# Performance work log

Measured on AMD Instinct MI355X. Metric: run time of the kernel, lower is better.

Reference implementation:

```python
import jax, jax.numpy as jnp
import numpy as np

N_E = 1024
E_DIM = 64


def setup_inputs() -> dict:
    key = jax.random.key(0)
    k_z, k_emb = jax.random.split(key)
    z = jax.random.normal(k_z, (8, 16, 32, 32, E_DIM), dtype=jnp.float32)
    embeddings = jax.random.normal(k_emb, (N_E, E_DIM), dtype=jnp.float32) * 0.02
    return {"z": z, "embeddings": embeddings}


def reference(z, embeddings):
    # flatten all leading dims: [B*T*H*W, e_dim]
    zf = z.reshape(-1, z.shape[-1])
    # squared L2 distance: ||z||^2 + ||e||^2 - 2 z.e  -> [tokens, n_e]
    d = (jnp.sum(zf ** 2, axis=1, keepdims=True)
         + jnp.sum(embeddings ** 2, axis=1)[None, :]
         - 2.0 * jnp.einsum('bd,nd->bn', zf, embeddings))
    idx = jnp.argmin(d, axis=1)
    z_q = embeddings[idx].reshape(z.shape)
    idx = idx.reshape(z.shape[:-1])
    return z_q, idx
```

## Files before the change

kernel.cpp:

```cpp
#include <hip/hip_runtime.h>

typedef short short8 __attribute__((ext_vector_type(8)));
typedef float f32x4 __attribute__((ext_vector_type(4)));

#define NTOK (8 * 16 * 32 * 32)
#define NE 1024
#define ED 64
#define TPB 256
#define MBLK 128
#define NMF 2
#define WKEY (1 << 18)
#define SCALE (-131072.0f)

__device__ __forceinline__ unsigned short bf16_rtne(float f) {
    unsigned u = __float_as_uint(f);
    return (unsigned short)((u + 0x7FFFu + ((u >> 16) & 1u)) >> 16);
}
__device__ __forceinline__ float bf16_to_f32(unsigned short h) {
    return __uint_as_float(((unsigned)h) << 16);
}

__device__ float exact_dist(const float* __restrict__ z, const float* __restrict__ emb,
                            int t, int e) {
    const float* zt = z + (size_t)t * ED;
    const float* ep = emb + (size_t)e * ED;
    float r0 = 0.f, r1 = 0.f, r2 = 0.f, r3 = 0.f;
    float r4 = 0.f, r5 = 0.f, r6 = 0.f, r7 = 0.f;
    for (int d = 0; d < ED; d += 8) {
        r0 += zt[d + 0] * zt[d + 0];
        r1 += zt[d + 1] * zt[d + 1];
        r2 += zt[d + 2] * zt[d + 2];
        r3 += zt[d + 3] * zt[d + 3];
        r4 += zt[d + 4] * zt[d + 4];
        r5 += zt[d + 5] * zt[d + 5];
        r6 += zt[d + 6] * zt[d + 6];
        r7 += zt[d + 7] * zt[d + 7];
    }
    float s1 = ((r0 + r1) + (r2 + r3)) + ((r4 + r5) + (r6 + r7));
    float q0 = 0.f, q1 = 0.f, q2 = 0.f, q3 = 0.f;
    float q4 = 0.f, q5 = 0.f, q6 = 0.f, q7 = 0.f;
    for (int d = 0; d < ED; d += 8) {
        float v0 = ep[d + 0], v1 = ep[d + 1], v2 = ep[d + 2], v3 = ep[d + 3];
        float v4 = ep[d + 4], v5 = ep[d + 5], v6 = ep[d + 6], v7 = ep[d + 7];
        q0 += v0 * v0; q1 += v1 * v1; q2 += v2 * v2; q3 += v3 * v3;
        q4 += v4 * v4; q5 += v5 * v5; q6 += v6 * v6; q7 += v7 * v7;
    }
    float s2 = ((q0 + q1) + (q2 + q3)) + ((q4 + q5) + (q6 + q7));
    float a0 = 0.f, a1 = 0.f, a2 = 0.f, a3 = 0.f;
    for (int d = 0; d < ED; d += 4) {
        a0 = fmaf(zt[d + 0], ep[d + 0], a0);
        a1 = fmaf(zt[d + 1], ep[d + 1], a1);
        a2 = fmaf(zt[d + 2], ep[d + 2], a2);
        a3 = fmaf(zt[d + 3], ep[d + 3], a3);
    }
    float g = (a0 + a1) + (a2 + a3);
    return (s1 + s2) - 2.0f * g;
}

__global__ __launch_bounds__(128) void vq_prep(
    const float* __restrict__ emb,
    unsigned short* __restrict__ bfH,
    unsigned short* __restrict__ bfL,
    float* __restrict__ s2s)
{
    const int f = blockIdx.x * 128 + threadIdx.x;
    const int col = f & 15;
    const int quad = (f >> 4) & 3;
    const int kb = (f >> 6) & 1;
    const int nt = f >> 7;
    const int e = nt * 16 + col;
    const int k0 = kb * 32 + quad * 8;

    const float* p = emb + (size_t)e * ED + k0;
    float4 v0 = *(const float4*)p;
    float4 v1 = *(const float4*)(p + 4);
    float vs[8] = {v0.x, v0.y, v0.z, v0.w, v1.x, v1.y, v1.z, v1.w};
    short8 h, l;
#pragma unroll
    for (int j = 0; j < 8; ++j) {
        float x = vs[j] * SCALE;
        unsigned short hb = bf16_rtne(x);
        float hf = bf16_to_f32(hb);
        unsigned short lb = bf16_rtne(x - hf);
        h[j] = (short)hb;
        l[j] = (short)lb;
    }
    *(short8*)&bfH[(size_t)f * 8] = h;
    *(short8*)&bfL[(size_t)f * 8] = l;

    if (f < 4096) {
        const int row = f >> 2;
        const float4* rp = (const float4*)(emb + (size_t)row * ED + (f & 3) * 16);
        float4 a = rp[0], b = rp[1], c = rp[2], d = rp[3];
        float s = a.x * a.x + a.y * a.y + a.z * a.z + a.w * a.w
                + b.x * b.x + b.y * b.y + b.z * b.z + b.w * b.w
                + c.x * c.x + c.y * c.y + c.z * c.z + c.w * c.w
                + d.x * d.x + d.y * d.y + d.z * d.z + d.w * d.w;
        s += __shfl_xor(s, 1);
        s += __shfl_xor(s, 2);
        if ((f & 3) == 0) s2s[row] = s * 65536.0f;
    }
}

__global__ void __launch_bounds__(TPB)
__attribute__((amdgpu_waves_per_eu(4, 4))) vq_main(
    const float* __restrict__ z,
    const float* __restrict__ emb,
    const unsigned short* __restrict__ bfH,
    const unsigned short* __restrict__ bfL,
    const float* __restrict__ s2s_g,
    float* __restrict__ zq_out,
    float* __restrict__ idx_out)
{
    __shared__ float s2L[NE];
    __shared__ int idx_lds[MBLK];
    __shared__ uint4 Bbuf[2][256];

    const int tid = threadIdx.x;
    const int lane = tid & 63;
    const int wv = __builtin_amdgcn_readfirstlane(tid >> 6);
    const int col = lane & 15;
    const int quad = lane >> 4;
    const int blockTok = blockIdx.x * MBLK;

    for (int i = tid; i < NE; i += TPB) s2L[i] = s2s_g[i];

    const uint4* src = (const uint4*)(tid < 128 ? bfH : bfL);
    const int chunk = tid & 127;
    const int dstc = (tid >> 7) * 128 + chunk;

    short8 Ah[NMF][2], Al[NMF][2];
#pragma unroll
    for (int mf = 0; mf < NMF; ++mf) {
#pragma unroll
        for (int kf = 0; kf < 2; ++kf) {
            const float* zp = z + (size_t)(blockTok + wv * 32 + mf * 16 + col) * ED
                              + kf * 32 + quad * 8;
            float4 v0 = *(const float4*)zp;
            float4 v1 = *(const float4*)(zp + 4);
            float vs[8] = {v0.x, v0.y, v0.z, v0.w, v1.x, v1.y, v1.z, v1.w};
            short8 h, l;
#pragma unroll
            for (int j = 0; j < 8; ++j) {
                float x = vs[j];
                unsigned short hb = bf16_rtne(x);
                float hf = bf16_to_f32(hb);
                unsigned short lb = bf16_rtne(x - hf);
                h[j] = (short)hb;
                l[j] = (short)lb;
            }
            Ah[mf][kf] = h;
            Al[mf][kf] = l;
        }
    }

    int aK[NMF][4], bK[NMF][4];
#pragma unroll
    for (int mf = 0; mf < NMF; ++mf)
#pragma unroll
        for (int r = 0; r < 4; ++r) { aK[mf][r] = 0x7FFFFFFF; bK[mf][r] = 0x7FFFFFFF; }

    Bbuf[0][dstc] = src[chunk];
    __syncthreads();

    int p = 0;
    for (int nt = 0; nt < 64; ++nt) {
        uint4 nv;
        if (nt < 63) nv = src[(nt + 1) * 128 + chunk];

        const short8* bp = (const short8*)Bbuf[p];
        short8 Bh0 = bp[lane];
        short8 Bh1 = bp[64 + lane];
        short8 Bl0 = bp[128 + lane];
        short8 Bl1 = bp[192 + lane];

        const float s2v = s2L[nt * 16 + col];
        const int e = nt * 16 + col;
#pragma unroll
        for (int mf = 0; mf < NMF; ++mf) {
            f32x4 cc = {s2v, s2v, s2v, s2v};
            cc = __builtin_amdgcn_mfma_f32_16x16x32_bf16(Ah[mf][0], Bh0, cc, 0, 0, 0);
            cc = __builtin_amdgcn_mfma_f32_16x16x32_bf16(Ah[mf][1], Bh1, cc, 0, 0, 0);
            cc = __builtin_amdgcn_mfma_f32_16x16x32_bf16(Al[mf][0], Bh0, cc, 0, 0, 0);
            cc = __builtin_amdgcn_mfma_f32_16x16x32_bf16(Al[mf][1], Bh1, cc, 0, 0, 0);
            cc = __builtin_amdgcn_mfma_f32_16x16x32_bf16(Ah[mf][0], Bl0, cc, 0, 0, 0);
            cc = __builtin_amdgcn_mfma_f32_16x16x32_bf16(Ah[mf][1], Bl1, cc, 0, 0, 0);
#pragma unroll
            for (int r = 0; r < 4; ++r) {
                int key = ((int)cc[r]) * 1024 + e;
                int t1 = min(aK[mf][r], key);
                bK[mf][r] = min(bK[mf][r], max(aK[mf][r], key));
                aK[mf][r] = t1;
            }
        }

        if (nt < 63) Bbuf[p ^ 1][dstc] = nv;
        __syncthreads();
        p ^= 1;
    }

#pragma unroll
    for (int mf = 0; mf < NMF; ++mf) {
#pragma unroll
        for (int r = 0; r < 4; ++r) {
            const int a0 = aK[mf][r], b0 = bK[mf][r];
            int A = a0, B = b0;
#pragma unroll
            for (int off = 1; off < 16; off <<= 1) {
                int A2 = __shfl_xor(A, off);
                int B2 = __shfl_xor(B, off);
                int lo = min(A, A2), hi = max(A, A2);
                B = min(min(B, B2), hi);
                A = lo;
            }
            int winner = A & 1023;
            if (B - A <= WKEY) {
                const int t = blockTok + wv * 32 + mf * 16 + quad * 4 + r;
                float dbest = 3.4e38f;
                int ibest = 1 << 30;
                if (a0 <= A + WKEY) {
                    int e = a0 & 1023;
                    float d = exact_dist(z, emb, t, e);
                    if (d < dbest || (d == dbest && e < ibest)) { dbest = d; ibest = e; }
                }
                if (b0 <= A + WKEY) {
                    int e = b0 & 1023;
                    float d = exact_dist(z, emb, t, e);
                    if (d < dbest || (d == dbest && e < ibest)) { dbest = d; ibest = e; }
                }
#pragma unroll
                for (int off = 1; off < 16; off <<= 1) {
                    float d2 = __shfl_xor(dbest, off);
                    int i2 = __shfl_xor(ibest, off);
                    if (d2 < dbest || (d2 == dbest && i2 < ibest)) { dbest = d2; ibest = i2; }
                }
                winner = ibest;
            }
            if (col == 0) idx_lds[wv * 32 + mf * 16 + quad * 4 + r] = winner;
        }
    }

    __syncthreads();

    if (tid < MBLK) idx_out[blockTok + tid] = (float)idx_lds[tid];
    const float4* emb_f4 = (const float4*)emb;
    float4* zq_f4 = (float4*)zq_out;
#pragma unroll
    for (int i = 0; i < MBLK * 16 / TPB; ++i) {
        int item = tid + i * TPB;
        int tl = item >> 4, f4 = item & 15;
        int wi = idx_lds[tl];
        zq_f4[(size_t)(blockTok + tl) * 16 + f4] = emb_f4[(size_t)wi * 16 + f4];
    }
}

extern "C" void kernel_launch(void* const* d_in, const int* in_sizes, int n_in,
                              void* d_out, int out_size, void* d_ws, size_t ws_size,
                              hipStream_t stream) {
    const float* z = (const float*)d_in[0];
    const float* emb = (const float*)d_in[1];
    float* out = (float*)d_out;
    float* zq = out;
    float* idx = out + (size_t)NTOK * ED;

    char* ws = (char*)d_ws;
    float* s2s = (float*)ws;
    unsigned short* bfH = (unsigned short*)(ws + 4096);
    unsigned short* bfL = (unsigned short*)(ws + 4096 + 131072);

    vq_prep<<<64, 128, 0, stream>>>(emb, bfH, bfL, s2s);
    vq_main<<<NTOK / MBLK, TPB, 0, stream>>>(z, emb, bfH, bfL, s2s, zq, idx);
}
```

Measured before the change: 152.0 us.

## Load codebook tiles directly into registers and use v_med3 for top-2 update

Removes the shared-memory double buffer and per-tile __syncthreads. Each wave now loads its B fragments straight from global memory (through L1/L2) into registers, prefetching the next tile. The second-best update becomes a single v_med3_i32, and the waves_per_eu upper bound is relaxed. The cost is 4x redundant global loads across the four waves and higher register use.

```diff
diff --git a/kernel.cpp b/kernel.cpp
--- a/kernel.cpp
+++ b/kernel.cpp
@@ -103,7 +103,7 @@
 }
 
 __global__ void __launch_bounds__(TPB)
-__attribute__((amdgpu_waves_per_eu(4, 4))) vq_main(
+__attribute__((amdgpu_waves_per_eu(4))) vq_main(
     const float* __restrict__ z,
     const float* __restrict__ emb,
     const unsigned short* __restrict__ bfH,
@@ -114,7 +114,6 @@
 {
     __shared__ float s2L[NE];
     __shared__ int idx_lds[MBLK];
-    __shared__ uint4 Bbuf[2][256];
 
     const int tid = threadIdx.x;
     const int lane = tid & 63;
@@ -124,10 +123,6 @@
     const int blockTok = blockIdx.x * MBLK;
 
     for (int i = tid; i < NE; i += TPB) s2L[i] = s2s_g[i];
-
-    const uint4* src = (const uint4*)(tid < 128 ? bfH : bfL);
-    const int chunk = tid & 127;
-    const int dstc = (tid >> 7) * 128 + chunk;
 
     short8 Ah[NMF][2], Al[NMF][2];
 #pragma unroll
@@ -160,19 +155,27 @@
 #pragma unroll
         for (int r = 0; r < 4; ++r) { aK[mf][r] = 0x7FFFFFFF; bK[mf][r] = 0x7FFFFFFF; }
 
-    Bbuf[0][dstc] = src[chunk];
+    const uint4* u4H = (const uint4*)bfH;
+    const uint4* u4L = (const uint4*)bfL;
+
+    uint4 cB0 = u4H[lane];
+    uint4 cB1 = u4H[64 + lane];
+    uint4 cB2 = u4L[lane];
+    uint4 cB3 = u4L[64 + lane];
+
     __syncthreads();
 
-    int p = 0;
     for (int nt = 0; nt < 64; ++nt) {
-        uint4 nv;
-        if (nt < 63) nv = src[(nt + 1) * 128 + chunk];
-
-        const short8* bp = (const short8*)Bbuf[p];
-        short8 Bh0 = bp[lane];
-        short8 Bh1 = bp[64 + lane];
-        short8 Bl0 = bp[128 + lane];
-        short8 Bl1 = bp[192 + lane];
+        const int nb = (((nt + 1) & 63) << 7) + lane;
+        uint4 nB0 = u4H[nb];
+        uint4 nB1 = u4H[nb + 64];
+        uint4 nB2 = u4L[nb];
+        uint4 nB3 = u4L[nb + 64];
+
+        short8 Bh0 = __builtin_bit_cast(short8, cB0);
+        short8 Bh1 = __builtin_bit_cast(short8, cB1);
+        short8 Bl0 = __builtin_bit_cast(short8, cB2);
+        short8 Bl1 = __builtin_bit_cast(short8, cB3);
 
         const float s2v = s2L[nt * 16 + col];
         const int e = nt * 16 + col;
@@ -188,15 +191,17 @@
 #pragma unroll
             for (int r = 0; r < 4; ++r) {
                 int key = ((int)cc[r]) * 1024 + e;
-                int t1 = min(aK[mf][r], key);
-                bK[mf][r] = min(bK[mf][r], max(aK[mf][r], key));
+                const int a0 = aK[mf][r];
+                int t1 = min(a0, key);
+                int med;
+                asm("v_med3_i32 %0, %1, %2, %3"
+                    : "=v"(med) : "v"(a0), "v"(bK[mf][r]), "v"(key));
+                bK[mf][r] = med;
                 aK[mf][r] = t1;
             }
         }
 
-        if (nt < 63) Bbuf[p ^ 1][dstc] = nv;
-        __syncthreads();
-        p ^= 1;
+        cB0 = nB0; cB1 = nB1; cB2 = nB2; cB3 = nB3;
     }
 
 #pragma unroll
```

Result: slower. 155.6 us (+2.4%).
